# Kernel optimization log

Hardware: AMD Instinct MI355X
Metric: run time of the kernel (lower is better)

## Reference

```python
import jax, jax.numpy as jnp
import numpy as np

N = 100_000   # n_unique_nodes
E = 200_000   # temporal edges
MEM = 172     # memory_dim == node feature dim
FEAT = 172
TD = 100      # time encoding dim
K = 10        # n_degree sampled neighbors
H = 2         # attention heads
DH = MEM // H
MSG = 2 * MEM + FEAT + TD  # identity message dim = 616


def setup_inputs() -> dict:
    key = jax.random.key(0)
    ks = jax.random.split(key, 24)
    s = 0.05
    return {
        "node_features": jax.random.normal(ks[0], (N, FEAT), jnp.float32),
        "memory": jax.random.normal(ks[1], (N, MEM), jnp.float32) * 0.1,
        "last_update": jnp.zeros((N,), jnp.float32),
        "timestamps": jnp.sort(jax.random.uniform(ks[2], (E,), jnp.float32) * 1e4),
        "edge_features": jax.random.normal(ks[3], (E, FEAT), jnp.float32),
        "neighbor_ts": jax.random.uniform(ks[4], (N, K), jnp.float32) * 1e4,
        "time_w": jax.random.normal(ks[5], (TD,), jnp.float32),
        "time_b": jax.random.normal(ks[6], (TD,), jnp.float32),
        "gru_Wi": jax.random.normal(ks[7], (3 * MEM, MSG), jnp.float32) * s,
        "gru_Wh": jax.random.normal(ks[8], (3 * MEM, MEM), jnp.float32) * s,
        "gru_bi": jnp.zeros((3 * MEM,), jnp.float32),
        "gru_bh": jnp.zeros((3 * MEM,), jnp.float32),
        "Wq": jax.random.normal(ks[9], (MEM + TD, MEM), jnp.float32) * s,
        "Wk": jax.random.normal(ks[10], (MEM + TD, MEM), jnp.float32) * s,
        "Wv": jax.random.normal(ks[11], (MEM + TD, MEM), jnp.float32) * s,
        "W1": jax.random.normal(ks[12], (2 * MEM, MEM), jnp.float32) * s,
        "b1": jnp.zeros((MEM,), jnp.float32),
        "W2": jax.random.normal(ks[13], (MEM, MEM), jnp.float32) * s,
        "b2": jnp.zeros((MEM,), jnp.float32),
        "fc2_w": jax.random.normal(ks[14], (MEM, 2), jnp.float32) * s,
        "fc2_b": jnp.zeros((2,), jnp.float32),
        "sources": jax.random.randint(ks[15], (E,), 0, N),
        "destinations": jax.random.randint(ks[16], (E,), 0, N),
        "neighbor_idx": jax.random.randint(ks[17], (N, K), 0, N),
    }


def reference(node_features, memory, last_update, timestamps, edge_features,
              neighbor_ts, time_w, time_b, gru_Wi, gru_Wh, gru_bi, gru_bh,
              Wq, Wk, Wv, W1, b1, W2, b2, fc2_w, fc2_b,
              sources, destinations, neighbor_idx):
    tenc = lambda t: jnp.cos(t[..., None] * time_w + time_b)  # [..., TD]

    # ---- identity messages for both endpoints of each temporal edge ----
    mem_s, mem_d = memory[sources], memory[destinations]
    dts = timestamps - last_update[sources]
    dtd = timestamps - last_update[destinations]
    msg_s = jnp.concatenate([mem_s, mem_d, edge_features, tenc(dts)], axis=1)
    msg_d = jnp.concatenate([mem_d, mem_s, edge_features, tenc(dtd)], axis=1)
    msgs = jnp.concatenate([msg_s, msg_d], axis=0)          # [2E, MSG]
    node_ids = jnp.concatenate([sources, destinations])      # [2E]
    ts2 = jnp.concatenate([timestamps, timestamps])

    # ---- 'last' aggregator: keep most recent message per node ----
    pos = jnp.arange(2 * E, dtype=jnp.int32)
    last_pos = jax.ops.segment_max(pos, node_ids, num_segments=N)
    has_msg = last_pos >= 0                                  # empty segs -> int min
    safe = jnp.maximum(last_pos, 0)
    m = msgs[safe]                                           # [N, MSG]
    t_node = ts2[safe]

    # ---- GRU memory updater ----
    gi = m @ gru_Wi.T + gru_bi
    gh = memory @ gru_Wh.T + gru_bh
    r = jax.nn.sigmoid(gi[:, :MEM] + gh[:, :MEM])
    z = jax.nn.sigmoid(gi[:, MEM:2 * MEM] + gh[:, MEM:2 * MEM])
    n = jnp.tanh(gi[:, 2 * MEM:] + r * gh[:, 2 * MEM:])
    h_new = (1.0 - z) * n + z * memory
    memory_upd = jnp.where(has_msg[:, None], h_new, memory)  # [N, MEM]

    # ---- temporal graph attention embedding (1 layer, H heads, K neighbors) ----
    h = memory_upd + node_features                           # [N, MEM]
    t_now = timestamps[-1]
    q_in = jnp.concatenate([h, tenc(jnp.zeros((N,), h.dtype))], axis=1)   # [N, MEM+TD]
    n_h = h[neighbor_idx]                                    # [N, K, MEM]
    k_in = jnp.concatenate([n_h, tenc(t_now - neighbor_ts)], axis=2)     # [N, K, MEM+TD]
    q = (q_in @ Wq).reshape(N, H, DH)
    k = (k_in @ Wk).reshape(N, K, H, DH)
    v = (k_in @ Wv).reshape(N, K, H, DH)
    scores = jnp.einsum('nhd,nkhd->nhk', q, k) / np.sqrt(DH).astype(np.float32)
    attn = jax.nn.softmax(scores, axis=-1)
    agg = jnp.einsum('nhk,nkhd->nhd', attn, v).reshape(N, MEM)
    emb = jnp.maximum(jnp.concatenate([h, agg], axis=1) @ W1 + b1, 0.0) @ W2 + b2

    # ---- classifier head (visible part of Net.forward) ----
    out_feature = jnp.mean(emb[1:], axis=0)                  # skip padding node 0
    logits = jnp.tanh(out_feature) @ fc2_w + fc2_b
    return jax.nn.softmax(logits.reshape(1, -1), axis=1)
```

## Files before the change

kernel.cpp:

```cpp
#include <hip/hip_runtime.h>
#include <hip/hip_bf16.h>
#include <math.h>

#define NND 100000
#define NED 200000
#define MROWS 100096

using bf16 = __hip_bfloat16;
using short8 = __attribute__((ext_vector_type(8))) short;
using short4v = __attribute__((ext_vector_type(4))) short;
using f32x4  = __attribute__((ext_vector_type(4))) float;

typedef __attribute__((address_space(3))) void lds_t;
typedef __attribute__((address_space(1))) const void gv_t;
__device__ __forceinline__ void gl16(const void* g, void* l) {
  __builtin_amdgcn_global_load_lds((gv_t*)g, (lds_t*)l, 16, 0, 0);
}

__device__ __forceinline__ float bfs2f(short s) {
  union { unsigned u; float f; } v; v.u = ((unsigned)(unsigned short)s) << 16; return v.f;
}
__device__ __forceinline__ short f2bfs(float f) {
  bf16 b = __float2bfloat16(f);
  union { bf16 b; short s; } u; u.b = b; return u.s;
}

#define INV2PI 0.15915494309189533577f

__device__ __forceinline__ float cos_rev(float r) {
  r = r - floorf(r);
  return __builtin_amdgcn_cosf(r);
}
__device__ __forceinline__ float fast_exp(float x) { return __expf(x); }
__device__ __forceinline__ float fast_rcp(float x) { return __builtin_amdgcn_rcpf(x); }
__device__ __forceinline__ float fast_sigmoid(float x) {
  return __builtin_amdgcn_rcpf(1.f + __expf(-x));
}
__device__ __forceinline__ float fast_tanh(float x) {
  float e = __expf(2.f * fabsf(x));
  float t = 1.f - 2.f * __builtin_amdgcn_rcpf(e + 1.f);
  return copysignf(t, x);
}


__global__ void init_k(int* lastpos, float* relu_sum, const float* __restrict__ tw,
                       const float* __restrict__ tb, float* twp, float* tbp) {
  int i = blockIdx.x * 256 + threadIdx.x;
  if (i < NND) lastpos[i] = -1;
  if (i < 172) relu_sum[i] = 0.f;
  if (i < 128) {
    twp[i] = (i < 100) ? tw[i] * INV2PI : 0.f;
    tbp[i] = (i < 100) ? tb[i] * INV2PI : 0.f;
  }
}

__global__ void scatter_k(const int* __restrict__ src, const int* __restrict__ dst,
                          int* lastpos) {
  int e = blockIdx.x * 256 + threadIdx.x;
  if (e < NED) {
    atomicMax(&lastpos[src[e]], e);
    atomicMax(&lastpos[dst[e]], NED + e);
  }
}

__global__ void meta_k(const int* __restrict__ lastpos,
                       const int* __restrict__ src, const int* __restrict__ dst,
                       const float* __restrict__ ts, const float* __restrict__ last_update,
                       int* other, int* edge, float* dtv, int* hasm) {
  int n = blockIdx.x * 256 + threadIdx.x;
  if (n >= NND) return;
  int p = lastpos[n];
  int oth = n, e = 0, hm = 0;
  float d = 0.f;
  if (p >= 0) {
    hm = 1;
    if (p >= NED) { e = p - NED; oth = src[e]; }
    else          { e = p;       oth = dst[e]; }
    d = ts[e] - last_update[n];
  }
  other[n] = oth; edge[n] = e; dtv[n] = d; hasm[n] = hm;
}

__global__ void qbias_k(const float* __restrict__ tb, const float* __restrict__ Wq,
                        float* qbias) {
  int o = threadIdx.x;
  if (o < 172) {
    float s = 0.f;
    for (int d = 0; d < 100; d++) s += cosf(tb[d]) * Wq[(172 + d) * 172 + o];
    qbias[o] = s;
  }
}

__global__ void bias716_k(const float* __restrict__ qbias, const float* __restrict__ Wk,
                          float* bias) {
  int o = blockIdx.x * 256 + threadIdx.x;
  if (o >= 716) return;
  float v = 0.f;
  if (o < 172) v = qbias[o];
  else if (o >= 516) {
    int p = o - 516, hh = p / 100, d = p - hh * 100;
    const float* qb  = qbias + hh * 86;
    const float* wk2 = Wk + (172 + d) * 172 + hh * 86;
    float s = 0.f;
    for (int cc = 0; cc < 86; cc++) s = fmaf(qb[cc], wk2[cc], s);
    v = s;
  }
  bias[o] = v;
}

__global__ void cvtW_k(const float* __restrict__ src, bf16* __restrict__ dst,
                       int R, int S, int r, int s) {
  int i = blockIdx.x * 256 + threadIdx.x;
  if (i >= R * S) return;
  int rr = i / S, cc = i - rr * S;
  float v = (rr < r && cc < s) ? src[(size_t)rr * s + cc] : 0.f;
  dst[i] = __float2bfloat16(v);
}

__global__ void packBT_k(const float* __restrict__ Wq, const float* __restrict__ Wk,
                         const float* __restrict__ Wv, bf16* __restrict__ dst) {
  int i = blockIdx.x * 256 + threadIdx.x;
  if (i >= 768 * 192) return;
  int o = i / 192, c = i - o * 192;
  float v = 0.f;
  if (o < 716 && c < 172) {
    if (o < 172)      v = Wq[c * 172 + o];
    else if (o < 344) v = Wk[c * 172 + (o - 172)];
    else if (o < 516) v = Wv[c * 172 + (o - 344)];
    else {
      int p = o - 516, hh = p / 100, d = p - hh * 100;
      const float* wq  = Wq + c * 172 + hh * 86;
      const float* wk2 = Wk + (172 + d) * 172 + hh * 86;
      float s = 0.f;
      for (int cc = 0; cc < 86; cc++) s = fmaf(wq[cc], wk2[cc], s);
      v = s;
    }
  }
  dst[i] = __float2bfloat16(v);
}

__global__ void packW1x_k(const float* __restrict__ W1, const float* __restrict__ Wv,
                          bf16* __restrict__ dst) {
  int i = blockIdx.x * 256 + threadIdx.x;
  if (i >= 256 * 544) return;
  int o = i / 544, k = i - o * 544;
  float v = 0.f;
  if (o < 172) {
    if (k < 344) v = W1[(size_t)k * 172 + o];
    else {
      int p = k - 344, hh = p / 100, d = p - hh * 100;
      const float* wv2 = Wv + (size_t)(172 + d) * 172;
      float s = 0.f;
      for (int t = hh * 86; t < hh * 86 + 86; t++)
        s = fmaf(wv2[t], W1[(size_t)(172 + t) * 172 + o], s);
      v = s;
    }
  }
  dst[i] = __float2bfloat16(v);
}

__global__ void msg2_k(const float* __restrict__ mem, const float* __restrict__ ef,
                       const int* __restrict__ other, const int* __restrict__ edge,
                       const float* __restrict__ dtv, const float* __restrict__ twp,
                       const float* __restrict__ tbp, bf16* __restrict__ Mg) {
  int i = blockIdx.x * 256 + threadIdx.x;
  if (i >= MROWS * 80) return;
  int n = i / 80, c8 = i - n * 80;
  int c = c8 * 8;
  short8 st = {0, 0, 0, 0, 0, 0, 0, 0};
  if (n < NND && c < 616) {
    float v[8];
    if (c + 8 <= 172) {
      float4 a = *(const float4*)(mem + (size_t)n * 172 + c);
      float4 b = *(const float4*)(mem + (size_t)n * 172 + c + 4);
      v[0]=a.x; v[1]=a.y; v[2]=a.z; v[3]=a.w; v[4]=b.x; v[5]=b.y; v[6]=b.z; v[7]=b.w;
    } else if (c >= 176 && c + 8 <= 344) {
      const float* src = mem + (size_t)other[n] * 172 + (c - 172);
      float4 a = *(const float4*)(src);
      float4 b = *(const float4*)(src + 4);
      v[0]=a.x; v[1]=a.y; v[2]=a.z; v[3]=a.w; v[4]=b.x; v[5]=b.y; v[6]=b.z; v[7]=b.w;
    } else if (c >= 344 && c + 8 <= 516) {
      const float* src = ef + (size_t)edge[n] * 172 + (c - 344);
      float4 a = *(const float4*)(src);
      float4 b = *(const float4*)(src + 4);
      v[0]=a.x; v[1]=a.y; v[2]=a.z; v[3]=a.w; v[4]=b.x; v[5]=b.y; v[6]=b.z; v[7]=b.w;
    } else if (c >= 520) {
      float d0 = dtv[n];
      #pragma unroll
      for (int p = 0; p < 8; p++)
        v[p] = cos_rev(fmaf(d0, twp[c - 516 + p], tbp[c - 516 + p]));
    } else {
      float d0 = dtv[n];
      #pragma unroll
      for (int p = 0; p < 8; p++) {
        int col = c + p;
        float x;
        if (col < 172)      x = mem[(size_t)n * 172 + col];
        else if (col < 344) x = mem[(size_t)other[n] * 172 + (col - 172)];
        else if (col < 516) x = ef[(size_t)edge[n] * 172 + (col - 344)];
        else                x = cos_rev(fmaf(d0, twp[col - 516], tbp[col - 516]));
        v[p] = x;
      }
    }
    #pragma unroll
    for (int p = 0; p < 8; p++) st[p] = f2bfs(v[p]);
  }
  *(short8*)(Mg + (size_t)n * 640 + c) = st;
}

__global__ void cvtmem_k(const float* __restrict__ mem, bf16* __restrict__ dst) {
  int i = blockIdx.x * 256 + threadIdx.x;
  if (i >= MROWS * 192) return;
  int n = i / 192, c = i - n * 192;
  float v = (n < NND && c < 172) ? mem[(size_t)n * 172 + c] : 0.f;
  dst[i] = __float2bfloat16(v);
}

__global__ void padrow_k(bf16* __restrict__ haw) {
  int i = blockIdx.x * 256 + threadIdx.x;
  if (i < (MROWS - NND) * 544) haw[(size_t)NND * 544 + i] = __float2bfloat16(0.f);
}

__global__ void padkv_k(bf16* __restrict__ kv) {
  int i = blockIdx.x * 256 + threadIdx.x;
  if (i >= NND * 21) return;
  int n = i / 21, c8 = i - n * 21;
  short8 z = {0, 0, 0, 0, 0, 0, 0, 0};
  *(short8*)(kv + (size_t)n * 512 + 344 + 8 * c8) = z;
}

__global__ void gru2_k(const bf16* __restrict__ gi, const bf16* __restrict__ gh,
                       const float* __restrict__ memory, const float* __restrict__ nf,
                       const int* __restrict__ hasm,
                       bf16* __restrict__ hB, bf16* __restrict__ haw) {
  int i = blockIdx.x * 256 + threadIdx.x;
  if (i >= MROWS * 48) return;
  int n = i / 48, c = (i - n * 48) * 4;
  short4v z4 = {0, 0, 0, 0};
  if (n >= NND || c >= 172) {
    *(short4v*)(hB + (size_t)n * 192 + c) = z4;
    return;
  }
  float4 mv = *(const float4*)(memory + (size_t)n * 172 + c);
  float hv[4] = {mv.x, mv.y, mv.z, mv.w};
  if (hasm[n]) {
    const bf16* gin = gi + (size_t)n * 516 + c;
    const bf16* ghn = gh + (size_t)n * 516 + c;
    short4v g0 = *(const short4v*)(gin);
    short4v g1 = *(const short4v*)(gin + 172);
    short4v g2 = *(const short4v*)(gin + 344);
    short4v h0 = *(const short4v*)(ghn);
    short4v h1 = *(const short4v*)(ghn + 172);
    short4v h2 = *(const short4v*)(ghn + 344);
    #pragma unroll
    for (int p = 0; p < 4; p++) {
      float r  = fast_sigmoid(bfs2f(g0[p]) + bfs2f(h0[p]));
      float zz = fast_sigmoid(bfs2f(g1[p]) + bfs2f(h1[p]));
      float nn = fast_tanh(bfs2f(g2[p]) + r * bfs2f(h2[p]));
      hv[p] = (1.f - zz) * nn + zz * hv[p];
    }
  }
  float4 nfv = *(const float4*)(nf + (size_t)n * 172 + c);
  float nfa[4] = {nfv.x, nfv.y, nfv.z, nfv.w};
  short4v hb;
  #pragma unroll
  for (int p = 0; p < 4; p++) hb[p] = f2bfs(hv[p] + nfa[p]);
  *(short4v*)(hB + (size_t)n * 192 + c) = hb;
  *(short4v*)(haw + (size_t)n * 544 + c) = hb;
}


template<int EPI>
__global__ __launch_bounds__(256) void mgemm_k(
    const bf16* __restrict__ A, int AS, const bf16* __restrict__ B, int BS,
    const float* __restrict__ bias,
    float* __restrict__ C, int CS, bf16* __restrict__ Cb, int CbS,
    float* __restrict__ red, int M, int O, int K) {
  __shared__ bf16 As[128 * 32];
  __shared__ bf16 Bs[128 * 32];
  const int tid = threadIdx.x, w = tid >> 6, lane = tid & 63;
  const int m0 = blockIdx.y * 128, o0 = blockIdx.x * 128;
  const int quad = lane >> 4, l16 = lane & 15;
  const int wm = (w & 1) * 64, wn = (w >> 1) * 64;
  f32x4 acc[4][4] = {};
  const bf16* ga = A + (size_t)(m0 + w * 32 + (lane >> 2)) * AS + (lane & 3) * 8;
  const bf16* gb = B + (size_t)(o0 + w * 32 + (lane >> 2)) * BS + (lane & 3) * 8;
  bf16* lA = As + w * 1024;
  bf16* lB = Bs + w * 1024;
  for (int k0 = 0; k0 < K; k0 += 32) {
    gl16(ga, lA);               gl16(ga + (size_t)16 * AS, lA + 512);
    gl16(gb, lB);               gl16(gb + (size_t)16 * BS, lB + 512);
    ga += 32; gb += 32;
    __syncthreads();
    short8 af[4], bfm[4];
    #pragma unroll
    for (int i = 0; i < 4; i++)
      af[i] = *(const short8*)&As[(wm + i * 16 + l16) * 32 + quad * 8];
    #pragma unroll
    for (int j = 0; j < 4; j++)
      bfm[j] = *(const short8*)&Bs[(wn + j * 16 + l16) * 32 + quad * 8];
    #pragma unroll
    for (int i = 0; i < 4; i++)
      #pragma unroll
      for (int j = 0; j < 4; j++)
        acc[i][j] = __builtin_amdgcn_mfma_f32_16x16x32_bf16(af[i], bfm[j], acc[i][j], 0, 0, 0);
    __syncthreads();
  }
  if (EPI == 2) {
    #pragma unroll
    for (int i = 0; i < 4; i++)
      #pragma unroll
      for (int p = 0; p < 4; p++) {
        const int m = m0 + wm + i * 16 + quad * 4 + p;
        if (m < M) {
          #pragma unroll
          for (int j = 0; j < 4; j++) {
            const int o = o0 + wn + j * 16 + l16;
            if (o < O) Cb[(size_t)m * CbS + o] = __float2bfloat16(acc[i][j][p] + bias[o]);
          }
        }
      }
  } else if (EPI == 3) {
    #pragma unroll
    for (int i = 0; i < 4; i++)
      #pragma unroll
      for (int p = 0; p < 4; p++) {
        const int m = m0 + wm + i * 16 + quad * 4 + p;
        if (m < M) {
          #pragma unroll
          for (int j = 0; j < 4; j++) {
            const int o = o0 + wn + j * 16 + l16;
            if (o < O) {
              const float v = acc[i][j][p] + bias[o];
              if (o < 172)      C[(size_t)m * CS + o] = v;
              else if (o < 516) Cb[(size_t)m * CbS + (o - 172)] = __float2bfloat16(v);
              else              C[(size_t)m * CS + (o - 344)] = v;
            }
          }
        }
      }
  } else {
    __shared__ float colsum[128];
    if (tid < 128) colsum[tid] = 0.f;
    __syncthreads();
    float part[4] = {0.f, 0.f, 0.f, 0.f};
    #pragma unroll
    for (int i = 0; i < 4; i++)
      #pragma unroll
      for (int p = 0; p < 4; p++) {
        const int m = m0 + wm + i * 16 + quad * 4 + p;
        const bool valid = (m < M) && (m != 0);
        if (valid) {
          #pragma unroll
          for (int j = 0; j < 4; j++) {
            const int o = o0 + wn + j * 16 + l16;
            if (o < O) part[j] += fmaxf(acc[i][j][p] + bias[o], 0.f);
          }
        }
      }
    #pragma unroll
    for (int j = 0; j < 4; j++) atomicAdd(&colsum[wn + j * 16 + l16], part[j]);
    __syncthreads();
    if (tid < 128) {
      const int o = o0 + tid;
      if (o < O) atomicAdd(&red[o], colsum[tid]);
    }
  }
}

__global__ __launch_bounds__(256) void attn4_k(
    const float* __restrict__ Cq, const bf16* __restrict__ kv,
    const float* __restrict__ twp, const float* __restrict__ tbp,
    const int* __restrict__ nidx, const float* __restrict__ nts,
    const float* __restrict__ ts, bf16* __restrict__ haw) {
  const int w = threadIdx.x >> 6, lane = threadIdx.x & 63;
  const int wid = __builtin_amdgcn_readfirstlane(blockIdx.x * 4 + w);
  const float t_now = ts[NED - 1];

  int ixs[10]; float ndt[10];
  #pragma unroll
  for (int j = 0; j < 10; j++) ixs[j] = nidx[wid * 10 + j];
  #pragma unroll
  for (int j = 0; j < 10; j++) ndt[j] = t_now - nts[wid * 10 + j];

  short8 kvc[10];
  #pragma unroll
  for (int j = 0; j < 10; j++)
    kvc[j] = *(const short8*)(kv + (size_t)ixs[j] * 512 + 8 * lane);

  const float* row = Cq + (size_t)wid * 372;
  float qs0[8], qs1[8];
  {
    float qc[8];
    if (lane < 22) {
      float4 a = *(const float4*)(row + 8 * lane);
      float4 b = *(const float4*)(row + 8 * lane + 4);
      qc[0] = a.x; qc[1] = a.y; qc[2] = a.z; qc[3] = a.w;
      qc[4] = b.x; qc[5] = b.y; qc[6] = b.z; qc[7] = b.w;
    } else {
      #pragma unroll
      for (int p = 0; p < 8; p++) qc[p] = 0.f;
    }
    #pragma unroll
    for (int p = 0; p < 8; p++) {
      const int e = 8 * lane + p;
      qs0[p] = (e < 86) ? qc[p] : 0.f;
      qs1[p] = (e >= 86 && e < 172) ? qc[p] : 0.f;
    }
  }
  const float k0a = row[172 + lane];
  const float k0b_raw = row[236 + lane];
  const float k1a = row[272 + lane];
  const float k1b_raw = row[336 + lane];
  const bool ln36 = (lane < 36);
  const float k0b = ln36 ? k0b_raw : 0.f;
  const float k1b = ln36 ? k1b_raw : 0.f;
  const float twa = twp[lane],      tba = tbp[lane];
  const float twb = twp[64 + lane], tbb = tbp[64 + lane];

  float ta[10], tbv[10];
  #pragma unroll
  for (int j = 0; j < 10; j++) {
    ta[j]  = cos_rev(fmaf(ndt[j], twa, tba));
    tbv[j] = cos_rev(fmaf(ndt[j], twb, tbb));
  }

  float s0[10], s1[10];
  #pragma unroll
  for (int j = 0; j < 10; j++) {
    float p0 = ta[j] * k0a + tbv[j] * k0b;
    float p1 = ta[j] * k1a + tbv[j] * k1b;
    #pragma unroll
    for (int p = 0; p < 8; p++) {
      const float hvv = bfs2f(kvc[j][p]);
      p0 = fmaf(qs0[p], hvv, p0);
      p1 = fmaf(qs1[p], hvv, p1);
    }
    #pragma unroll
    for (int off = 32; off; off >>= 1) {
      p0 += __shfl_xor(p0, off);
      p1 += __shfl_xor(p1, off);
    }
    const float scale = 0.10783277320343841f;
    s0[j] = p0 * scale; s1[j] = p1 * scale;
  }
  float m0 = s0[0], m1v = s1[0];
  #pragma unroll
  for (int j = 1; j < 10; j++) { m0 = fmaxf(m0, s0[j]); m1v = fmaxf(m1v, s1[j]); }
  float z0 = 0.f, z1 = 0.f;
  #pragma unroll
  for (int j = 0; j < 10; j++) {
    s0[j] = fast_exp(s0[j] - m0);  z0 += s0[j];
    s1[j] = fast_exp(s1[j] - m1v); z1 += s1[j];
  }
  const float i0 = fast_rcp(z0), i1 = fast_rcp(z1);
  float av0[8] = {}, av1[8] = {};
  float w0a = 0.f, w0b = 0.f, w1a = 0.f, w1b = 0.f;
  #pragma unroll
  for (int j = 0; j < 10; j++) {
    const float a0 = s0[j] * i0, a1 = s1[j] * i1;
    #pragma unroll
    for (int p = 0; p < 8; p++) {
      const float hvv = bfs2f(kvc[j][p]);
      av0[p] = fmaf(a0, hvv, av0[p]);
      av1[p] = fmaf(a1, hvv, av1[p]);
    }
    w0a = fmaf(a0, ta[j], w0a); w0b = fmaf(a0, tbv[j], w0b);
    w1a = fmaf(a1, ta[j], w1a); w1b = fmaf(a1, tbv[j], w1b);
  }
  bf16* hrow = haw + (size_t)wid * 544;
  if (lane >= 22 && lane < 43) {
    short8 st;
    #pragma unroll
    for (int p = 0; p < 8; p++) {
      const int e = 8 * lane + p;
      st[p] = f2bfs((e < 258) ? av0[p] : av1[p]);
    }
    *(short8*)(hrow + 8 * lane) = st;
  } else if (lane == 21) {
    #pragma unroll
    for (int p = 4; p < 8; p++) hrow[168 + p] = __float2bfloat16(av0[p]);
  }
  hrow[344 + lane] = __float2bfloat16(w0a);
  if (ln36) hrow[408 + lane] = __float2bfloat16(w0b);
  hrow[444 + lane] = __float2bfloat16(w1a);
  if (ln36) hrow[508 + lane] = __float2bfloat16(w1b);
}


__global__ void head_k(const float* __restrict__ relu_sum, const float* __restrict__ W2,
                       const float* __restrict__ b2, const float* __restrict__ fc2w,
                       const float* __restrict__ fc2b, float* out) {
  __shared__ float th[172];
  int t = threadIdx.x;
  if (t < 172) {
    float s = 0.f;
    for (int c = 0; c < 172; c++) s = fmaf(relu_sum[c], W2[c * 172 + t], s);
    s = s * (1.0f / 99999.0f) + b2[t];
    th[t] = tanhf(s);
  }
  __syncthreads();
  if (t == 0) {
    float l0 = fc2b[0], l1 = fc2b[1];
    for (int o = 0; o < 172; o++) {
      l0 = fmaf(th[o], fc2w[o * 2 + 0], l0);
      l1 = fmaf(th[o], fc2w[o * 2 + 1], l1);
    }
    float mx = fmaxf(l0, l1);
    float e0 = expf(l0 - mx), e1 = expf(l1 - mx);
    float inv = 1.f / (e0 + e1);
    out[0] = e0 * inv;
    out[1] = e1 * inv;
  }
}


extern "C" void kernel_launch(void* const* d_in, const int* in_sizes, int n_in,
                              void* d_out, int out_size, void* d_ws, size_t ws_size,
                              hipStream_t stream) {
  (void)in_sizes; (void)n_in; (void)out_size;
  const float* node_features = (const float*)d_in[0];
  const float* memory        = (const float*)d_in[1];
  const float* last_update   = (const float*)d_in[2];
  const float* timestamps    = (const float*)d_in[3];
  const float* edge_features = (const float*)d_in[4];
  const float* neighbor_ts   = (const float*)d_in[5];
  const float* time_w        = (const float*)d_in[6];
  const float* time_b        = (const float*)d_in[7];
  const float* gru_Wi        = (const float*)d_in[8];
  const float* gru_Wh        = (const float*)d_in[9];
  const float* gru_bi        = (const float*)d_in[10];
  const float* gru_bh        = (const float*)d_in[11];
  const float* Wq            = (const float*)d_in[12];
  const float* Wk            = (const float*)d_in[13];
  const float* Wv            = (const float*)d_in[14];
  const float* W1            = (const float*)d_in[15];
  const float* b1            = (const float*)d_in[16];
  const float* W2            = (const float*)d_in[17];
  const float* b2            = (const float*)d_in[18];
  const float* fc2_w         = (const float*)d_in[19];
  const float* fc2_b         = (const float*)d_in[20];
  const int* sources         = (const int*)d_in[21];
  const int* destinations    = (const int*)d_in[22];
  const int* neighbor_idx    = (const int*)d_in[23];
  float* out = (float*)d_out;

  float* F = (float*)d_ws;
  int*   I = (int*)d_ws;
  size_t off = 0;
  auto alloc = [&off](size_t words) { size_t r = off; off += (words + 63) & ~(size_t)63; return r; };
  const size_t w_lastpos = alloc(NND);
  const size_t w_other   = alloc(NND);
  const size_t w_edge    = alloc(NND);
  const size_t w_dtv     = alloc(NND);
  const size_t w_hasm    = alloc(NND);
  const size_t w_qbias   = alloc(172);
  const size_t w_b716    = alloc(716);
  const size_t w_relu    = alloc(172);
  const size_t w_twp     = alloc(128);
  const size_t w_tbp     = alloc(128);
  const size_t w_WiB     = alloc(640 * 640 / 2);
  const size_t w_WhB     = alloc(640 * 192 / 2);
  const size_t w_pBT     = alloc(768 * 192 / 2);
  const size_t w_W1x     = alloc(256 * 544 / 2);
  const size_t w_R1 = alloc((size_t)NND * 372 + 256);
  const size_t w_R2 = alloc((size_t)NND * 516 / 2);
  const size_t w_R4 = alloc((size_t)MROWS * 192 / 2);
  const size_t w_R5 = alloc((size_t)MROWS * 544 / 2);
  if (ws_size < off * 4) return;

  int*   lastpos = I + w_lastpos;
  int*   other   = I + w_other;
  int*   edge    = I + w_edge;
  float* dtv     = F + w_dtv;
  int*   hasm    = I + w_hasm;
  float* qbias   = F + w_qbias;
  float* b716    = F + w_b716;
  float* relu_s  = F + w_relu;
  float* twp     = F + w_twp;
  float* tbp     = F + w_tbp;
  bf16*  WiB     = (bf16*)(F + w_WiB);
  bf16*  WhB     = (bf16*)(F + w_WhB);
  bf16*  pBT     = (bf16*)(F + w_pBT);
  bf16*  W1x     = (bf16*)(F + w_W1x);
  bf16*  Mg      = (bf16*)(F + w_R1);
  bf16*  ghB     = (bf16*)(F + w_R1);
  float* Cq      = F + w_R1;
  bf16*  giB     = (bf16*)(F + w_R2);
  bf16*  kvB     = (bf16*)(F + w_R2);
  bf16*  memB    = (bf16*)(F + w_R4);
  bf16*  hB      = (bf16*)(F + w_R4);
  bf16*  haw     = (bf16*)(F + w_R5);

  init_k<<<(NND + 255) / 256, 256, 0, stream>>>(lastpos, relu_s, time_w, time_b, twp, tbp);
  scatter_k<<<(NED + 255) / 256, 256, 0, stream>>>(sources, destinations, lastpos);
  meta_k<<<(NND + 255) / 256, 256, 0, stream>>>(lastpos, sources, destinations,
                                                timestamps, last_update,
                                                other, edge, dtv, hasm);
  qbias_k<<<1, 256, 0, stream>>>(time_b, Wq, qbias);
  bias716_k<<<3, 256, 0, stream>>>(qbias, Wk, b716);
  cvtW_k<<<(640 * 640 + 255) / 256, 256, 0, stream>>>(gru_Wi, WiB, 640, 640, 516, 616);
  cvtW_k<<<(640 * 192 + 255) / 256, 256, 0, stream>>>(gru_Wh, WhB, 640, 192, 516, 172);
  packBT_k<<<(768 * 192 + 255) / 256, 256, 0, stream>>>(Wq, Wk, Wv, pBT);
  packW1x_k<<<(256 * 544 + 255) / 256, 256, 0, stream>>>(W1, Wv, W1x);
  msg2_k<<<(MROWS * 80) / 256, 256, 0, stream>>>(memory, edge_features, other, edge,
                                                 dtv, twp, tbp, Mg);
  cvtmem_k<<<(MROWS * 192) / 256, 256, 0, stream>>>(memory, memB);
  padrow_k<<<((MROWS - NND) * 544 + 255) / 256, 256, 0, stream>>>(haw);

  mgemm_k<2><<<dim3(5, 782), 256, 0, stream>>>(Mg, 640, WiB, 640, gru_bi,
                                               nullptr, 0, giB, 516, nullptr,
                                               NND, 516, 640);
  mgemm_k<2><<<dim3(5, 782), 256, 0, stream>>>(memB, 192, WhB, 192, gru_bh,
                                               nullptr, 0, ghB, 516, nullptr,
                                               NND, 516, 192);
  gru2_k<<<(MROWS * 48) / 256, 256, 0, stream>>>(giB, ghB, memory, node_features,
                                                 hasm, hB, haw);
  padkv_k<<<(NND * 21 + 255) / 256, 256, 0, stream>>>(kvB);
  mgemm_k<3><<<dim3(6, 782), 256, 0, stream>>>(hB, 192, pBT, 192, b716,
                                               Cq, 372, kvB, 512, nullptr,
                                               NND, 716, 192);
  attn4_k<<<NND / 4, 256, 0, stream>>>(Cq, kvB, twp, tbp,
                                       neighbor_idx, neighbor_ts, timestamps, haw);
  mgemm_k<1><<<dim3(2, 782), 256, 0, stream>>>(haw, 544, W1x, 544, b1,
                                               nullptr, 0, nullptr, 0, relu_s,
                                               NND, 172, 544);
  head_k<<<1, 256, 0, stream>>>(relu_s, W2, b2, fc2_w, fc2_b, out);
}
```

Before: 1.442 ms.

## Double-buffer GEMM LDS, store Cq in bf16, fuse kv padding, cut attention registers

The GEMM kernel now double-buffers its LDS tiles so the next K-slice load overlaps the MFMA work on the current one. The Q/K projection output Cq is written as bf16 instead of fp32, and the kv padding is zeroed inside the GEMM epilogue, which removes the separate padkv kernel. The attention kernel reloads neighbor kv rows and recomputes the time encodings in each pass instead of holding them in registers, and raises its occupancy hint. Storing Cq in bf16 loses some precision, and the second kv gather relies on cache hits.

```diff
diff --git a/kernel.cpp b/kernel.cpp
--- a/kernel.cpp
+++ b/kernel.cpp
@@ -221,14 +221,6 @@
   if (i < (MROWS - NND) * 544) haw[(size_t)NND * 544 + i] = __float2bfloat16(0.f);
 }
 
-__global__ void padkv_k(bf16* __restrict__ kv) {
-  int i = blockIdx.x * 256 + threadIdx.x;
-  if (i >= NND * 21) return;
-  int n = i / 21, c8 = i - n * 21;
-  short8 z = {0, 0, 0, 0, 0, 0, 0, 0};
-  *(short8*)(kv + (size_t)n * 512 + 344 + 8 * c8) = z;
-}
-
 __global__ void gru2_k(const bf16* __restrict__ gi, const bf16* __restrict__ gh,
                        const float* __restrict__ memory, const float* __restrict__ nf,
                        const int* __restrict__ hasm,
@@ -274,37 +266,44 @@
 __global__ __launch_bounds__(256) void mgemm_k(
     const bf16* __restrict__ A, int AS, const bf16* __restrict__ B, int BS,
     const float* __restrict__ bias,
-    float* __restrict__ C, int CS, bf16* __restrict__ Cb, int CbS,
+    bf16* __restrict__ Cq, int CqS, bf16* __restrict__ Cb, int CbS,
     float* __restrict__ red, int M, int O, int K) {
-  __shared__ bf16 As[128 * 32];
-  __shared__ bf16 Bs[128 * 32];
+  __shared__ bf16 As[2][128 * 32];
+  __shared__ bf16 Bs[2][128 * 32];
   const int tid = threadIdx.x, w = tid >> 6, lane = tid & 63;
   const int m0 = blockIdx.y * 128, o0 = blockIdx.x * 128;
   const int quad = lane >> 4, l16 = lane & 15;
   const int wm = (w & 1) * 64, wn = (w >> 1) * 64;
+  const int wo = w * 1024;
   f32x4 acc[4][4] = {};
   const bf16* ga = A + (size_t)(m0 + w * 32 + (lane >> 2)) * AS + (lane & 3) * 8;
   const bf16* gb = B + (size_t)(o0 + w * 32 + (lane >> 2)) * BS + (lane & 3) * 8;
-  bf16* lA = As + w * 1024;
-  bf16* lB = Bs + w * 1024;
-  for (int k0 = 0; k0 < K; k0 += 32) {
-    gl16(ga, lA);               gl16(ga + (size_t)16 * AS, lA + 512);
-    gl16(gb, lB);               gl16(gb + (size_t)16 * BS, lB + 512);
-    ga += 32; gb += 32;
-    __syncthreads();
+  gl16(ga, As[0] + wo);  gl16(ga + (size_t)16 * AS, As[0] + wo + 512);
+  gl16(gb, Bs[0] + wo);  gl16(gb + (size_t)16 * BS, Bs[0] + wo + 512);
+  ga += 32; gb += 32;
+  __syncthreads();
+  const int nt = K >> 5;
+  int cur = 0;
+  for (int t = 0; t < nt; ++t) {
+    if (t + 1 < nt) {
+      gl16(ga, As[cur ^ 1] + wo);  gl16(ga + (size_t)16 * AS, As[cur ^ 1] + wo + 512);
+      gl16(gb, Bs[cur ^ 1] + wo);  gl16(gb + (size_t)16 * BS, Bs[cur ^ 1] + wo + 512);
+      ga += 32; gb += 32;
+    }
     short8 af[4], bfm[4];
     #pragma unroll
     for (int i = 0; i < 4; i++)
-      af[i] = *(const short8*)&As[(wm + i * 16 + l16) * 32 + quad * 8];
+      af[i] = *(const short8*)&As[cur][(wm + i * 16 + l16) * 32 + quad * 8];
     #pragma unroll
     for (int j = 0; j < 4; j++)
-      bfm[j] = *(const short8*)&Bs[(wn + j * 16 + l16) * 32 + quad * 8];
+      bfm[j] = *(const short8*)&Bs[cur][(wn + j * 16 + l16) * 32 + quad * 8];
     #pragma unroll
     for (int i = 0; i < 4; i++)
       #pragma unroll
       for (int j = 0; j < 4; j++)
         acc[i][j] = __builtin_amdgcn_mfma_f32_16x16x32_bf16(af[i], bfm[j], acc[i][j], 0, 0, 0);
     __syncthreads();
+    cur ^= 1;
   }
   if (EPI == 2) {
     #pragma unroll
@@ -332,9 +331,12 @@
             const int o = o0 + wn + j * 16 + l16;
             if (o < O) {
               const float v = acc[i][j][p] + bias[o];
-              if (o < 172)      C[(size_t)m * CS + o] = v;
+              if (o < 172)      Cq[(size_t)m * CqS + o] = __float2bfloat16(v);
               else if (o < 516) Cb[(size_t)m * CbS + (o - 172)] = __float2bfloat16(v);
-              else              C[(size_t)m * CS + (o - 344)] = v;
+              else {
+                Cq[(size_t)m * CqS + (o - 344)] = __float2bfloat16(v);
+                if (o < 684) Cb[(size_t)m * CbS + (o - 172)] = __float2bfloat16(0.f);
+              }
             }
           }
         }
@@ -368,8 +370,8 @@
   }
 }
 
-__global__ __launch_bounds__(256) void attn4_k(
-    const float* __restrict__ Cq, const bf16* __restrict__ kv,
+__global__ __launch_bounds__(256, 8) void attn5_k(
+    const bf16* __restrict__ Cq, const bf16* __restrict__ kv,
     const float* __restrict__ twp, const float* __restrict__ tbp,
     const int* __restrict__ nidx, const float* __restrict__ nts,
     const float* __restrict__ ts, bf16* __restrict__ haw) {
@@ -383,56 +385,38 @@
   #pragma unroll
   for (int j = 0; j < 10; j++) ndt[j] = t_now - nts[wid * 10 + j];
 
-  short8 kvc[10];
-  #pragma unroll
-  for (int j = 0; j < 10; j++)
-    kvc[j] = *(const short8*)(kv + (size_t)ixs[j] * 512 + 8 * lane);
-
-  const float* row = Cq + (size_t)wid * 372;
+  const short* row = (const short*)Cq + (size_t)wid * 384;
   float qs0[8], qs1[8];
   {
-    float qc[8];
-    if (lane < 22) {
-      float4 a = *(const float4*)(row + 8 * lane);
-      float4 b = *(const float4*)(row + 8 * lane + 4);
-      qc[0] = a.x; qc[1] = a.y; qc[2] = a.z; qc[3] = a.w;
-      qc[4] = b.x; qc[5] = b.y; qc[6] = b.z; qc[7] = b.w;
-    } else {
-      #pragma unroll
-      for (int p = 0; p < 8; p++) qc[p] = 0.f;
-    }
+    short8 qc8 = {0, 0, 0, 0, 0, 0, 0, 0};
+    if (lane < 22) qc8 = *(const short8*)(row + 8 * lane);
     #pragma unroll
     for (int p = 0; p < 8; p++) {
       const int e = 8 * lane + p;
-      qs0[p] = (e < 86) ? qc[p] : 0.f;
-      qs1[p] = (e >= 86 && e < 172) ? qc[p] : 0.f;
-    }
-  }
-  const float k0a = row[172 + lane];
-  const float k0b_raw = row[236 + lane];
-  const float k1a = row[272 + lane];
-  const float k1b_raw = row[336 + lane];
+      const float v = bfs2f(qc8[p]);
+      qs0[p] = (e < 86) ? v : 0.f;
+      qs1[p] = (e >= 86 && e < 172) ? v : 0.f;
+    }
+  }
   const bool ln36 = (lane < 36);
-  const float k0b = ln36 ? k0b_raw : 0.f;
-  const float k1b = ln36 ? k1b_raw : 0.f;
+  const float k0a = bfs2f(row[172 + lane]);
+  const float k0b = ln36 ? bfs2f(row[236 + lane]) : 0.f;
+  const float k1a = bfs2f(row[272 + lane]);
+  const float k1b = ln36 ? bfs2f(row[336 + lane]) : 0.f;
   const float twa = twp[lane],      tba = tbp[lane];
   const float twb = twp[64 + lane], tbb = tbp[64 + lane];
-
-  float ta[10], tbv[10];
-  #pragma unroll
-  for (int j = 0; j < 10; j++) {
-    ta[j]  = cos_rev(fmaf(ndt[j], twa, tba));
-    tbv[j] = cos_rev(fmaf(ndt[j], twb, tbb));
-  }
 
   float s0[10], s1[10];
   #pragma unroll
   for (int j = 0; j < 10; j++) {
-    float p0 = ta[j] * k0a + tbv[j] * k0b;
-    float p1 = ta[j] * k1a + tbv[j] * k1b;
+    const short8 c = *(const short8*)(kv + (size_t)ixs[j] * 512 + 8 * lane);
+    const float tja = cos_rev(fmaf(ndt[j], twa, tba));
+    const float tjb = cos_rev(fmaf(ndt[j], twb, tbb));
+    float p0 = tja * k0a + tjb * k0b;
+    float p1 = tja * k1a + tjb * k1b;
     #pragma unroll
     for (int p = 0; p < 8; p++) {
-      const float hvv = bfs2f(kvc[j][p]);
+      const float hvv = bfs2f(c[p]);
       p0 = fmaf(qs0[p], hvv, p0);
       p1 = fmaf(qs1[p], hvv, p1);
     }
@@ -454,19 +438,23 @@
     s1[j] = fast_exp(s1[j] - m1v); z1 += s1[j];
   }
   const float i0 = fast_rcp(z0), i1 = fast_rcp(z1);
+
   float av0[8] = {}, av1[8] = {};
   float w0a = 0.f, w0b = 0.f, w1a = 0.f, w1b = 0.f;
   #pragma unroll
   for (int j = 0; j < 10; j++) {
+    const short8 c = *(const short8*)(kv + (size_t)ixs[j] * 512 + 8 * lane);
+    const float tja = cos_rev(fmaf(ndt[j], twa, tba));
+    const float tjb = cos_rev(fmaf(ndt[j], twb, tbb));
     const float a0 = s0[j] * i0, a1 = s1[j] * i1;
     #pragma unroll
     for (int p = 0; p < 8; p++) {
-      const float hvv = bfs2f(kvc[j][p]);
+      const float hvv = bfs2f(c[p]);
       av0[p] = fmaf(a0, hvv, av0[p]);
       av1[p] = fmaf(a1, hvv, av1[p]);
     }
-    w0a = fmaf(a0, ta[j], w0a); w0b = fmaf(a0, tbv[j], w0b);
-    w1a = fmaf(a1, ta[j], w1a); w1b = fmaf(a1, tbv[j], w1b);
+    w0a = fmaf(a0, tja, w0a); w0b = fmaf(a0, tjb, w0b);
+    w1a = fmaf(a1, tja, w1a); w1b = fmaf(a1, tjb, w1b);
   }
   bf16* hrow = haw + (size_t)wid * 544;
   if (lane >= 22 && lane < 43) {
@@ -585,7 +573,7 @@
   bf16*  W1x     = (bf16*)(F + w_W1x);
   bf16*  Mg      = (bf16*)(F + w_R1);
   bf16*  ghB     = (bf16*)(F + w_R1);
-  float* Cq      = F + w_R1;
+  bf16*  Cqb     = (bf16*)(F + w_R1);
   bf16*  giB     = (bf16*)(F + w_R2);
   bf16*  kvB     = (bf16*)(F + w_R2);
   bf16*  memB    = (bf16*)(F + w_R4);
@@ -616,11 +604,10 @@
                                                NND, 516, 192);
   gru2_k<<<(MROWS * 48) / 256, 256, 0, stream>>>(giB, ghB, memory, node_features,
                                                  hasm, hB, haw);
-  padkv_k<<<(NND * 21 + 255) / 256, 256, 0, stream>>>(kvB);
   mgemm_k<3><<<dim3(6, 782), 256, 0, stream>>>(hB, 192, pBT, 192, b716,
-                                               Cq, 372, kvB, 512, nullptr,
+                                               Cqb, 384, kvB, 512, nullptr,
                                                NND, 716, 192);
-  attn4_k<<<NND / 4, 256, 0, stream>>>(Cq, kvB, twp, tbp,
+  attn5_k<<<NND / 4, 256, 0, stream>>>(Cqb, kvB, twp, tbp,
                                        neighbor_idx, neighbor_ts, timestamps, haw);
   mgemm_k<1><<<dim3(2, 782), 256, 0, stream>>>(haw, 544, W1x, 544, b1,
                                                nullptr, 0, nullptr, 0, relu_s,
```

Measured after the change: 3.505 ms. 2.43x slower.
